# Kernel tuning notes

Hardware: AMD Instinct MI355X
Metric: run time of the kernel (lower is better)

## Reference

```python
import jax, jax.numpy as jnp
import numpy as np

S, B, H = 2048, 1, 1024
N_HEADS = 16
HEAD_DIM = H // N_HEADS
E, K, F = 8, 2, 2048  # experts, top_k, ffn_hidden
EPS = 1e-5


def layernorm(x, w, b):
    mu = jnp.mean(x, axis=-1, keepdims=True)
    var = jnp.mean(jnp.square(x - mu), axis=-1, keepdims=True)
    return (x - mu) * jax.lax.rsqrt(var + EPS) * w + b


def setup_inputs() -> dict:
    key = jax.random.key(0)
    ks = jax.random.split(key, 8)
    std = 0.02
    return {
        "x": jax.random.normal(ks[0], (S, B, H), dtype=jnp.float32),
        "ln1_w": jnp.ones((H,), jnp.float32),
        "ln1_b": jnp.zeros((H,), jnp.float32),
        "in_proj_w": jax.random.normal(ks[1], (3 * H, H), jnp.float32) * std,
        "in_proj_b": jnp.zeros((3 * H,), jnp.float32),
        "out_proj_w": jax.random.normal(ks[2], (H, H), jnp.float32) * std,
        "out_proj_b": jnp.zeros((H,), jnp.float32),
        "ln2_w": jnp.ones((H,), jnp.float32),
        "ln2_b": jnp.zeros((H,), jnp.float32),
        "router_w": jax.random.normal(ks[3], (E, H), jnp.float32) * std,
        "w1": jax.random.normal(ks[4], (E, H, F), jnp.float32) * std,
        "w2": jax.random.normal(ks[5], (E, F, H), jnp.float32) * std,
    }


def reference(x, ln1_w, ln1_b, in_proj_w, in_proj_b, out_proj_w, out_proj_b,
              ln2_w, ln2_b, router_w, w1, w2):
    s, b, h = x.shape
    # ---- causal self-attention (nn.MultiheadAttention math) ----
    hn = layernorm(x, ln1_w, ln1_b)
    qkv = hn @ in_proj_w.T + in_proj_b          # [S,B,3H]
    q, k, v = jnp.split(qkv, 3, axis=-1)
    q = q.reshape(s, b, N_HEADS, HEAD_DIM)
    k = k.reshape(s, b, N_HEADS, HEAD_DIM)
    v = v.reshape(s, b, N_HEADS, HEAD_DIM)
    scores = jnp.einsum('sbnd,tbnd->bnst', q, k) / np.sqrt(HEAD_DIM)
    causal = jnp.tril(jnp.ones((s, s), bool))
    scores = jnp.where(causal[None, None], scores, -jnp.inf)
    probs = jax.nn.softmax(scores, axis=-1)
    attn = jnp.einsum('bnst,tbnd->sbnd', probs, v).reshape(s, b, h)
    attn = attn @ out_proj_w.T + out_proj_b
    x1 = x + attn
    # ---- dMoE FFN: router softmax -> top-k gates -> expert GELU MLP ----
    hn2 = layernorm(x1, ln2_w, ln2_b).reshape(s * b, h)   # tokens [T,H]
    logits = hn2 @ router_w.T                              # [T,E]
    rp = jax.nn.softmax(logits, axis=-1)
    topw, topi = jax.lax.top_k(rp, K)                      # [T,K]
    gates = jnp.sum(jax.nn.one_hot(topi, E, dtype=hn2.dtype) * topw[..., None], axis=1)  # [T,E]
    hmid = jax.nn.gelu(jnp.einsum('th,ehf->tef', hn2, w1), approximate=False)  # [T,E,F]
    y = jnp.einsum('tef,efh->th', hmid * gates[:, :, None], w2)                # [T,H]
    return x1 + y.reshape(s, b, h)
```

## Files before the change

### kernel.cpp

```cpp
#include <hip/hip_runtime.h>

#define SL 2048
#define HID 1024
#define NHEAD 16
#define HD 64
#define NEXP 8
#define FF 2048
#define MAXTILE 40
#define MAXROWS (MAXTILE * 128)
#define CPAD 32

typedef short bf16x8 __attribute__((ext_vector_type(8)));
typedef float f32x4 __attribute__((ext_vector_type(4)));
typedef unsigned u32x4 __attribute__((ext_vector_type(4)));

__device__ __forceinline__ unsigned short f2bf(float f) {
  unsigned u = __builtin_bit_cast(unsigned, f);
  u += 0x7fffu + ((u >> 16) & 1u);
  return (unsigned short)(u >> 16);
}

__device__ __forceinline__ void gload16(const void* g, void* l) {
  __builtin_amdgcn_global_load_lds((const __attribute__((address_space(1))) void*)g,
                                   (__attribute__((address_space(3))) void*)l,
                                   16, 0, 0);
}

__device__ __forceinline__ void xcd_remap(int& bx, int& by) {
  const int nx = gridDim.x;
  const int nwg = nx * gridDim.y;
  const int L = by * nx + bx;
  const int per = nwg >> 3;
  const int Lp = (L & 7) * per + (L >> 3);
  bx = Lp % nx;
  by = Lp / nx;
}


#define PIPE_WAIT(i, NT)                                                     \
  if ((i) == (NT) - 1)                                                       \
    asm volatile("s_waitcnt vmcnt(0) lgkmcnt(0)" ::: "memory");              \
  else                                                                       \
    asm volatile("s_waitcnt vmcnt(4) lgkmcnt(0)" ::: "memory");              \
  __builtin_amdgcn_s_barrier();

#define GEMM_FRAGS_MFMA(CC)                                                  \
  bf16x8 af[4], bfr[4];                                                      \
  _Pragma("unroll")                                                          \
  for (int mt = 0; mt < 4; mt++)                                             \
    af[mt] = *reinterpret_cast<const bf16x8*>(                               \
        &Asm[CC][(wm + mt * 16 + la) * 32 + lk]);                            \
  _Pragma("unroll")                                                          \
  for (int nt = 0; nt < 4; nt++)                                             \
    bfr[nt] = *reinterpret_cast<const bf16x8*>(                              \
        &Bsm[CC][(wn + nt * 16 + la) * 32 + lk]);                            \
  __builtin_amdgcn_s_setprio(1);                                             \
  _Pragma("unroll")                                                          \
  for (int mt = 0; mt < 4; mt++)                                             \
    _Pragma("unroll")                                                        \
    for (int nt = 0; nt < 4; nt++)                                           \
      acc[mt][nt] =                                                          \
          __builtin_amdgcn_mfma_f32_16x16x32_bf16(af[mt], bfr[nt], acc[mt][nt], 0, 0, 0); \
  __builtin_amdgcn_s_setprio(0);

#define PIPE_ROT()                                                           \
  cc = (cc == 2) ? 0 : cc + 1;                                               \
  cs = (cs == 2) ? 0 : cs + 1;

template <int MODE>
__global__ __launch_bounds__(256) void gemm_bt(
    const unsigned short* __restrict__ A, const unsigned short* __restrict__ Bt,
    int M, int N, int Kstride, int Kloop,
    const float* __restrict__ bias,
    float* __restrict__ outf,
    unsigned short* __restrict__ q_out, unsigned short* __restrict__ k_out,
    unsigned short* __restrict__ vt_out)
{
  __shared__ unsigned short Asm[3][128 * 32];
  __shared__ unsigned short Bsm[3][128 * 32];
  int bx = blockIdx.x, by = blockIdx.y;
  xcd_remap(bx, by);
  const int tid = threadIdx.x;
  const int wave = tid >> 6;
  const int lane = tid & 63;
  const int m0 = by * 128;
  const int n0 = bx * 128;
  const int koff = blockIdx.z * Kloop;
  const int wm = (wave >> 1) * 64;
  const int wn = (wave & 1) * 64;
  const int la = lane & 15;
  const int lk = (lane >> 4) * 8;

  f32x4 acc[4][4] = {};

  const int srow = tid >> 2;
  const int skoff = (tid & 3) * 8;
  const unsigned short* Ag = A + (size_t)(m0 + srow) * Kstride + koff + skoff;
  const unsigned short* Bg = Bt + (size_t)(n0 + srow) * Kstride + koff + skoff;

  auto stage = [&](int s, int k0) {
    gload16(Ag + k0, &Asm[s][wave * 512]);
    gload16(Ag + (size_t)64 * Kstride + k0, &Asm[s][2048 + wave * 512]);
    gload16(Bg + k0, &Bsm[s][wave * 512]);
    gload16(Bg + (size_t)64 * Kstride + k0, &Bsm[s][2048 + wave * 512]);
  };

  stage(0, 0);
  stage(1, 32);
  const int NT = Kloop >> 5;
  int cc = 0, cs = 2;
  for (int i = 0; i < NT; ++i) {
    PIPE_WAIT(i, NT)
    if (i + 2 < NT) stage(cs, (i + 2) << 5);
    GEMM_FRAGS_MFMA(cc)
    PIPE_ROT()
  }

  const int lg = lane >> 4;
#pragma unroll
  for (int mt = 0; mt < 4; mt++) {
#pragma unroll
    for (int nt = 0; nt < 4; nt++) {
#pragma unroll
      for (int r = 0; r < 4; r++) {
        const int row = m0 + wm + mt * 16 + lg * 4 + r;
        const int col = n0 + wn + nt * 16 + la;
        float v = acc[mt][nt][r];
        if (MODE == 0) {
          v += bias[col];
          const int hh = (col & 1023) >> 6;
          const int dd = col & 63;
          const unsigned short bv = f2bf(v);
          if (col < 1024)
            q_out[(size_t)hh * SL * HD + (size_t)row * HD + dd] = bv;
          else if (col < 2048)
            k_out[(size_t)hh * SL * HD + (size_t)row * HD + dd] = bv;
          else
            vt_out[(size_t)hh * HD * SL + (size_t)dd * SL + row] = bv;
        } else {
          outf[(size_t)blockIdx.z * SL * HID + (size_t)row * HID + col] = v;
        }
      }
    }
  }
}

__global__ __launch_bounds__(256) void gemm_moe1(
    const unsigned short* __restrict__ A, const unsigned short* __restrict__ w1t,
    const int* __restrict__ perm, const float* __restrict__ gateg,
    const int* __restrict__ texp, const int* __restrict__ trow,
    unsigned short* __restrict__ hmidg)
{
  __shared__ unsigned short Asm[3][128 * 32];
  __shared__ unsigned short Bsm[3][128 * 32];
  int bx = blockIdx.x, by = blockIdx.y;
  xcd_remap(bx, by);
  const int e = texp[by];
  if (e < 0) return;
  const int row0 = trow[by];
  const int tid = threadIdx.x;
  const int wave = tid >> 6;
  const int lane = tid & 63;
  const int n0 = bx * 128;
  const int wm = (wave >> 1) * 64;
  const int wn = (wave & 1) * 64;
  const int la = lane & 15;
  const int lk = (lane >> 4) * 8;
  f32x4 acc[4][4] = {};

  const int srow = tid >> 2;
  const int skoff = (tid & 3) * 8;
  const int p0 = perm[row0 + srow];
  const int p1 = perm[row0 + 64 + srow];
  const unsigned short* Ag0 = A + (size_t)(p0 < 0 ? 0 : (p0 >> 1)) * HID + skoff;
  const unsigned short* Ag1 = A + (size_t)(p1 < 0 ? 0 : (p1 >> 1)) * HID + skoff;
  const unsigned short* Bg = w1t + (size_t)e * HID * FF + (size_t)(n0 + srow) * HID + skoff;

  auto stage = [&](int s, int k0) {
    gload16(Ag0 + k0, &Asm[s][wave * 512]);
    gload16(Ag1 + k0, &Asm[s][2048 + wave * 512]);
    gload16(Bg + k0, &Bsm[s][wave * 512]);
    gload16(Bg + (size_t)64 * HID + k0, &Bsm[s][2048 + wave * 512]);
  };

  stage(0, 0);
  stage(1, 32);
  const int NT = HID >> 5;
  int cc = 0, cs = 2;
  for (int i = 0; i < NT; ++i) {
    PIPE_WAIT(i, NT)
    if (i + 2 < NT) stage(cs, (i + 2) << 5);
    GEMM_FRAGS_MFMA(cc)
    PIPE_ROT()
  }

  const int lg = lane >> 4;
#pragma unroll
  for (int mt = 0; mt < 4; mt++) {
    float gr[4];
#pragma unroll
    for (int r = 0; r < 4; r++) gr[r] = gateg[row0 + wm + mt * 16 + lg * 4 + r];
#pragma unroll
    for (int nt = 0; nt < 4; nt++) {
#pragma unroll
      for (int r = 0; r < 4; r++) {
        const int grow = row0 + wm + mt * 16 + lg * 4 + r;
        const int col = n0 + wn + nt * 16 + la;
        const float v = acc[mt][nt][r];
        const float g = 0.5f * v * (1.0f + erff(v * 0.70710678118f));
        hmidg[(size_t)grow * FF + col] = f2bf(g * gr[r]);
      }
    }
  }
}

__global__ __launch_bounds__(256) void gemm_moe2(
    const unsigned short* __restrict__ A, const unsigned short* __restrict__ w2t,
    const int* __restrict__ perm,
    const int* __restrict__ texp, const int* __restrict__ trow,
    float* __restrict__ ybuf)
{
  __shared__ unsigned short Asm[3][128 * 32];
  __shared__ unsigned short Bsm[3][128 * 32];
  int bx = blockIdx.x, by = blockIdx.y;
  xcd_remap(bx, by);
  const int e = texp[by];
  if (e < 0) return;
  const int row0 = trow[by];
  const int tid = threadIdx.x;
  const int wave = tid >> 6;
  const int lane = tid & 63;
  const int n0 = bx * 128;
  const int koff = blockIdx.z * (FF / 2);
  const int wm = (wave >> 1) * 64;
  const int wn = (wave & 1) * 64;
  const int la = lane & 15;
  const int lk = (lane >> 4) * 8;
  f32x4 acc[4][4] = {};

  const int srow = tid >> 2;
  const int skoff = (tid & 3) * 8;
  const unsigned short* Ag = A + (size_t)(row0 + srow) * FF + koff + skoff;
  const unsigned short* Bg = w2t + (size_t)e * FF * HID + (size_t)(n0 + srow) * FF + koff + skoff;

  auto stage = [&](int s, int k0) {
    gload16(Ag + k0, &Asm[s][wave * 512]);
    gload16(Ag + (size_t)64 * FF + k0, &Asm[s][2048 + wave * 512]);
    gload16(Bg + k0, &Bsm[s][wave * 512]);
    gload16(Bg + (size_t)64 * FF + k0, &Bsm[s][2048 + wave * 512]);
  };

  stage(0, 0);
  stage(1, 32);
  const int NT = (FF / 2) >> 5;
  int cc = 0, cs = 2;
  for (int i = 0; i < NT; ++i) {
    PIPE_WAIT(i, NT)
    if (i + 2 < NT) stage(cs, (i + 2) << 5);
    GEMM_FRAGS_MFMA(cc)
    PIPE_ROT()
  }

  const int lg = lane >> 4;
#pragma unroll
  for (int mt = 0; mt < 4; mt++) {
    int pr[4];
#pragma unroll
    for (int r = 0; r < 4; r++) pr[r] = perm[row0 + wm + mt * 16 + lg * 4 + r];
#pragma unroll
    for (int nt = 0; nt < 4; nt++) {
#pragma unroll
      for (int r = 0; r < 4; r++) {
        const int p = pr[r];
        if (p >= 0) {
          const int col = n0 + wn + nt * 16 + la;
          ybuf[(size_t)(blockIdx.z * 2 + (p & 1)) * SL * HID + (size_t)(p >> 1) * HID + col] =
              acc[mt][nt][r];
        }
      }
    }
  }
}

__global__ __launch_bounds__(256) void ln_kernel(
    const float* __restrict__ x, const float* __restrict__ w, const float* __restrict__ b,
    unsigned short* __restrict__ ob)
{
  const int row = blockIdx.x;
  const int tid = threadIdx.x;
  const float4 v = *reinterpret_cast<const float4*>(&x[(size_t)row * HID + tid * 4]);
  float s = v.x + v.y + v.z + v.w;
  float q = v.x * v.x + v.y * v.y + v.z * v.z + v.w * v.w;
  for (int off = 32; off > 0; off >>= 1) {
    s += __shfl_down(s, off);
    q += __shfl_down(q, off);
  }
  __shared__ float ps[4], pq[4];
  const int wave = tid >> 6, lane = tid & 63;
  if (lane == 0) { ps[wave] = s; pq[wave] = q; }
  __syncthreads();
  s = ps[0] + ps[1] + ps[2] + ps[3];
  q = pq[0] + pq[1] + pq[2] + pq[3];
  const float mu = s * (1.0f / HID);
  const float inv = rsqrtf(q * (1.0f / HID) - mu * mu + 1e-5f);
  const int i = tid * 4;
  const float4 wv = *reinterpret_cast<const float4*>(&w[i]);
  const float4 bv = *reinterpret_cast<const float4*>(&b[i]);
  ushort4 u;
  u.x = f2bf((v.x - mu) * inv * wv.x + bv.x);
  u.y = f2bf((v.y - mu) * inv * wv.y + bv.y);
  u.z = f2bf((v.z - mu) * inv * wv.z + bv.z);
  u.w = f2bf((v.w - mu) * inv * wv.w + bv.w);
  *reinterpret_cast<ushort4*>(&ob[(size_t)row * HID + i]) = u;
}

__global__ __launch_bounds__(256) void combine_ln(
    const float4* __restrict__ x, const float* __restrict__ bias,
    const float4* __restrict__ p0, const float4* __restrict__ p1,
    float4* __restrict__ x1,
    const float* __restrict__ w, const float* __restrict__ b,
    unsigned short* __restrict__ ob, float* __restrict__ of)
{
  const int row = blockIdx.x;
  const int tid = threadIdx.x;
  const int i4 = row * 256 + tid;
  const int i = tid * 4;
  const float4 bv0 = *reinterpret_cast<const float4*>(&bias[i]);
  const float4 a = x[i4], c = p0[i4], d = p1[i4];
  float4 v;
  v.x = a.x + bv0.x + c.x + d.x;
  v.y = a.y + bv0.y + c.y + d.y;
  v.z = a.z + bv0.z + c.z + d.z;
  v.w = a.w + bv0.w + c.w + d.w;
  x1[i4] = v;
  float s = v.x + v.y + v.z + v.w;
  float q = v.x * v.x + v.y * v.y + v.z * v.z + v.w * v.w;
  for (int off = 32; off > 0; off >>= 1) {
    s += __shfl_down(s, off);
    q += __shfl_down(q, off);
  }
  __shared__ float ps[4], pq[4];
  const int wave = tid >> 6, lane = tid & 63;
  if (lane == 0) { ps[wave] = s; pq[wave] = q; }
  __syncthreads();
  s = ps[0] + ps[1] + ps[2] + ps[3];
  q = pq[0] + pq[1] + pq[2] + pq[3];
  const float mu = s * (1.0f / HID);
  const float inv = rsqrtf(q * (1.0f / HID) - mu * mu + 1e-5f);
  const float4 wv = *reinterpret_cast<const float4*>(&w[i]);
  const float4 bv = *reinterpret_cast<const float4*>(&b[i]);
  const float o0 = (v.x - mu) * inv * wv.x + bv.x;
  const float o1 = (v.y - mu) * inv * wv.y + bv.y;
  const float o2 = (v.z - mu) * inv * wv.z + bv.z;
  const float o3 = (v.w - mu) * inv * wv.w + bv.w;
  ushort4 u; u.x = f2bf(o0); u.y = f2bf(o1); u.z = f2bf(o2); u.w = f2bf(o3);
  *reinterpret_cast<ushort4*>(&ob[(size_t)row * HID + i]) = u;
  float4 o; o.x = o0; o.y = o1; o.z = o2; o.w = o3;
  *reinterpret_cast<float4*>(&of[(size_t)row * HID + i]) = o;
}

__global__ __launch_bounds__(256) void transpose_all(
    const float* __restrict__ w1, const float* __restrict__ w2,
    unsigned short* __restrict__ w1t, unsigned short* __restrict__ w2t)
{
  __shared__ float t[64][65];
  const int z = blockIdx.z;
  const float* in;
  unsigned short* out;
  int R, C, r0, c0;
  if (z < 8) {
    in = w1 + (size_t)z * HID * FF;  out = w1t + (size_t)z * HID * FF;
    R = HID; C = FF;  r0 = blockIdx.y * 64;  c0 = blockIdx.x * 64;
  } else {
    in = w2 + (size_t)(z - 8) * FF * HID;  out = w2t + (size_t)(z - 8) * FF * HID;
    R = FF; C = HID;  r0 = blockIdx.x * 64;  c0 = blockIdx.y * 64;
  }
  const int tid = threadIdx.x;
#pragma unroll
  for (int it = 0; it < 4; it++) {
    const int idx = it * 256 + tid;
    const int r = idx >> 4, c4 = (idx & 15) * 4;
    const float4 v = *reinterpret_cast<const float4*>(&in[(size_t)(r0 + r) * C + c0 + c4]);
    t[r][c4] = v.x; t[r][c4 + 1] = v.y; t[r][c4 + 2] = v.z; t[r][c4 + 3] = v.w;
  }
  __syncthreads();
#pragma unroll
  for (int it = 0; it < 4; it++) {
    const int idx = it * 256 + tid;
    const int c = idx >> 4, r4 = (idx & 15) * 4;
    ushort4 u;
    u.x = f2bf(t[r4][c]); u.y = f2bf(t[r4 + 1][c]);
    u.z = f2bf(t[r4 + 2][c]); u.w = f2bf(t[r4 + 3][c]);
    *reinterpret_cast<ushort4*>(&out[(size_t)(c0 + c) * R + r0 + r4]) = u;
  }
}

__global__ __launch_bounds__(256) void conv_bf16_2(
    const float4* __restrict__ a, const float4* __restrict__ b,
    ushort4* __restrict__ oa, ushort4* __restrict__ ob, int na4, int nb4)
{
  const int i = blockIdx.x * 256 + threadIdx.x;
  if (i < na4) {
    const float4 v = a[i];
    ushort4 u; u.x = f2bf(v.x); u.y = f2bf(v.y); u.z = f2bf(v.z); u.w = f2bf(v.w);
    oa[i] = u;
  } else if (i - na4 < nb4) {
    const float4 v = b[i - na4];
    ushort4 u; u.x = f2bf(v.x); u.y = f2bf(v.y); u.z = f2bf(v.z); u.w = f2bf(v.w);
    ob[i - na4] = u;
  }
}

__global__ __launch_bounds__(256) void router_kernel(
    const float* __restrict__ hn2f, const float* __restrict__ rw,
    int* __restrict__ ti, float* __restrict__ tg, int* __restrict__ cnt)
{
  __shared__ float wlds[NEXP * HID];
  __shared__ int lcnt[NEXP];
  const int tid = threadIdx.x;
#pragma unroll
  for (int i = 0; i < 8; i++)
    *reinterpret_cast<float4*>(&wlds[i * 1024 + tid * 4]) =
        *reinterpret_cast<const float4*>(&rw[i * 1024 + tid * 4]);
  if (tid < NEXP) lcnt[tid] = 0;
  __syncthreads();

  const int wave = tid >> 6, lane = tid & 63;
#pragma unroll 1
  for (int k = 0; k < 4; k++) {
    const int t = blockIdx.x * 16 + wave * 4 + k;
    float4 xr[4];
#pragma unroll
    for (int c = 0; c < 4; c++)
      xr[c] = *reinterpret_cast<const float4*>(&hn2f[(size_t)t * HID + c * 256 + lane * 4]);
    float p[NEXP];
#pragma unroll
    for (int e = 0; e < NEXP; e++) {
      float s = 0.f;
#pragma unroll
      for (int c = 0; c < 4; c++) {
        const float4 wv = *reinterpret_cast<const float4*>(&wlds[e * 1024 + c * 256 + lane * 4]);
        s += xr[c].x * wv.x + xr[c].y * wv.y + xr[c].z * wv.z + xr[c].w * wv.w;
      }
      s += __shfl_xor(s, 32);
      s += __shfl_xor(s, 16);
      s += __shfl_xor(s, 8);
      s += __shfl_xor(s, 4);
      s += __shfl_xor(s, 2);
      s += __shfl_xor(s, 1);
      p[e] = s;
    }
    if (lane == 0) {
      float mx = p[0];
#pragma unroll
      for (int e = 1; e < NEXP; e++) mx = fmaxf(mx, p[e]);
      float Z = 0.f;
#pragma unroll
      for (int e = 0; e < NEXP; e++) { p[e] = expf(p[e] - mx); Z += p[e]; }
      const float invZ = 1.f / Z;
      int i1 = 0;
#pragma unroll
      for (int e = 1; e < NEXP; e++) if (p[e] > p[i1]) i1 = e;
      int i2 = (i1 == 0) ? 1 : 0;
#pragma unroll
      for (int e = 0; e < NEXP; e++) if (e != i1 && p[e] > p[i2]) i2 = e;
      ti[2 * t] = i1; ti[2 * t + 1] = i2;
      tg[2 * t] = p[i1] * invZ; tg[2 * t + 1] = p[i2] * invZ;
      atomicAdd(&lcnt[i1], 1);
      atomicAdd(&lcnt[i2], 1);
    }
  }
  __syncthreads();
  if (tid < NEXP && lcnt[tid] > 0) atomicAdd(&cnt[tid * CPAD], lcnt[tid]);
}

__global__ void scan_kernel(const int* __restrict__ cnt, int* __restrict__ poff,
                            int* __restrict__ texp, int* __restrict__ trow)
{
  if (threadIdx.x == 0 && blockIdx.x == 0) {
    int off = 0, nt = 0;
    for (int e = 0; e < NEXP; e++) {
      poff[e] = off;
      const int c = cnt[e * CPAD];
      const int ntl = (c + 127) >> 7;
      for (int i = 0; i < ntl; i++) { texp[nt] = e; trow[nt] = off + i * 128; nt++; }
      off += ntl * 128;
    }
    for (int i = nt; i < MAXTILE; i++) { texp[i] = -1; trow[i] = 0; }
  }
}

__global__ __launch_bounds__(256) void build_kernel(
    const int* __restrict__ ti, const float* __restrict__ tg,
    const int* __restrict__ poff, int* __restrict__ fill,
    int* __restrict__ perm, float* __restrict__ gateg)
{
  __shared__ int lcnt[NEXP], lbase[NEXP];
  const int tid = threadIdx.x;
  if (tid < NEXP) lcnt[tid] = 0;
  __syncthreads();
  const int t = blockIdx.x * 256 + tid;
  int e0 = ti[2 * t], e1 = ti[2 * t + 1];
  int l0 = atomicAdd(&lcnt[e0], 1);
  int l1 = atomicAdd(&lcnt[e1], 1);
  __syncthreads();
  if (tid < NEXP) lbase[tid] = (lcnt[tid] > 0) ? atomicAdd(&fill[tid * CPAD], lcnt[tid]) : 0;
  __syncthreads();
  int pos0 = poff[e0] + lbase[e0] + l0;
  int pos1 = poff[e1] + lbase[e1] + l1;
  perm[pos0] = 2 * t;
  gateg[pos0] = tg[2 * t];
  perm[pos1] = 2 * t + 1;
  gateg[pos1] = tg[2 * t + 1];
}

__global__ __launch_bounds__(256) void final_add(
    const float4* __restrict__ x1, const float4* __restrict__ y0,
    const float4* __restrict__ y1, const float4* __restrict__ y2,
    const float4* __restrict__ y3, float4* __restrict__ out)
{
  const int i = blockIdx.x * 256 + threadIdx.x;
  const float4 a = x1[i], b = y0[i], c = y1[i], d = y2[i], e = y3[i];
  float4 o;
  o.x = a.x + b.x + c.x + d.x + e.x;
  o.y = a.y + b.y + c.y + d.y + e.y;
  o.z = a.z + b.z + c.z + d.z + e.z;
  o.w = a.w + b.w + c.w + d.w + e.w;
  out[i] = o;
}

#define SC2 0.1803368801111204f
#define PPITCH 20
__global__ __launch_bounds__(512) void attn_kernel(
    const unsigned short* __restrict__ qb, const unsigned short* __restrict__ kb,
    const unsigned short* __restrict__ vtb, unsigned short* __restrict__ attn)
{
  const int h = blockIdx.y;
  const int tid = threadIdx.x;
  const int wave = tid >> 6, lane = tid & 63;
  const int grp = wave >> 2;
  const int w4 = wave & 3;
  const int la = lane & 15, lg = lane >> 4;
  const int la7 = la & 7;
  __shared__ unsigned short Kt[2][2][64 * 64];
  __shared__ unsigned short Vt[2][2][64 * 64];
  __shared__ unsigned plds[8 * 32 * PPITCH];
  const unsigned short* qh = qb + (size_t)h * SL * HD;
  const unsigned short* kh = kb + (size_t)h * SL * HD;
  const unsigned short* vh = vtb + (size_t)h * HD * SL;
  unsigned* pu = &plds[wave * 32 * PPITCH];

  const int sr_lo = w4 * 8 + (lane >> 3);
  const int ss = lane & 7;

  auto stageKV = [&](int t, int buf) {
    const int kvb = t * 64;
#pragma unroll
    for (int j = 0; j < 2; j++) {
      const int row = j * 32 + sr_lo;
      const int s = ss ^ (row & 7);
      gload16(kh + (size_t)(kvb + row) * HD + s * 8, &Kt[grp][buf][j * 2048 + w4 * 512]);
      gload16(vh + (size_t)row * SL + kvb + s * 8, &Vt[grp][buf][j * 2048 + w4 * 512]);
    }
  };

  for (int half = 0; half < 2; half++) {
    const int qt = half ? (31 - blockIdx.x) : blockIdx.x;
    const int m0 = qt * 64 + w4 * 16;
    const int T = qt + 1;
    const int S = (T + 1) >> 1;
    const int q = m0 + la;

    bf16x8 aq0 = *reinterpret_cast<const bf16x8*>(&qh[(size_t)(m0 + la) * HD + lg * 8]);
    bf16x8 aq1 = *reinterpret_cast<const bf16x8*>(&qh[(size_t)(m0 + la) * HD + 32 + lg * 8]);

    f32x4 oacc[4] = {};
    float mrun = -1e30f, lrun = 0.f;

    if (grp < T) stageKV(grp, 0);
    __syncthreads();
    int cur = 0;

    for (int s = 0; s < S; s++) {
      const int tmy = 2 * s + grp;
      if (tmy + 2 < T) stageKV(tmy + 2, cur ^ 1);
      if (tmy < T) {
        const int kv0 = tmy * 64;
        const unsigned short* Kb = Kt[grp][cur];
        const unsigned short* Vb = Vt[grp][cur];

        f32x4 sac[4] = {};
        __builtin_amdgcn_s_setprio(1);
#pragma unroll
        for (int nt = 0; nt < 4; nt++) {
          const int row = nt * 16 + la;
          bf16x8 b0 = *reinterpret_cast<const bf16x8*>(&Kb[row * 64 + ((lg ^ la7) << 3)]);
          bf16x8 b1 = *reinterpret_cast<const bf16x8*>(&Kb[row * 64 + (((4 + lg) ^ la7) << 3)]);
          sac[nt] = __builtin_amdgcn_mfma_f32_16x16x32_bf16(b0, aq0, sac[nt], 0, 0, 0);
          sac[nt] = __builtin_amdgcn_mfma_f32_16x16x32_bf16(b1, aq1, sac[nt], 0, 0, 0);
        }
        __builtin_amdgcn_s_setprio(0);
        float sv[4][4];
        const bool diag = (tmy == qt);
#pragma unroll
        for (int nt = 0; nt < 4; nt++)
#pragma unroll
          for (int r = 0; r < 4; r++) {
            float xs = sac[nt][r] * SC2;
            if (diag && (kv0 + nt * 16 + lg * 4 + r) > q) xs = -1e30f;
            sv[nt][r] = xs;
          }
        float pm = fmaxf(fmaxf(sv[0][0], sv[0][1]), fmaxf(sv[0][2], sv[0][3]));
#pragma unroll
        for (int nt = 1; nt < 4; nt++)
          pm = fmaxf(pm, fmaxf(fmaxf(sv[nt][0], sv[nt][1]), fmaxf(sv[nt][2], sv[nt][3])));
        pm = fmaxf(pm, __shfl_xor(pm, 16));
        pm = fmaxf(pm, __shfl_xor(pm, 32));
        const float mn = fmaxf(mrun, pm);
        float rs = 0.f;
#pragma unroll
        for (int nt = 0; nt < 4; nt++)
#pragma unroll
          for (int r = 0; r < 4; r++) {
            const float pe = exp2f(sv[nt][r] - mn);
            sv[nt][r] = pe;
            rs += pe;
          }
        rs += __shfl_xor(rs, 16);
        rs += __shfl_xor(rs, 32);
        if (__ballot(pm > mrun) != 0ULL) {
          const float al = exp2f(mrun - mn);
#pragma unroll
          for (int dt = 0; dt < 4; dt++)
#pragma unroll
            for (int r = 0; r < 4; r++) oacc[dt][r] *= al;
          lrun = lrun * al + rs;
          mrun = mn;
        } else {
          lrun += rs;
        }
#pragma unroll
        for (int nt = 0; nt < 4; nt++)
#pragma unroll
          for (int rp = 0; rp < 2; rp++) {
            unsigned pk;
            asm("v_cvt_pk_bf16_f32 %0, %1, %2"
                : "=v"(pk) : "v"(sv[nt][rp * 2]), "v"(sv[nt][rp * 2 + 1]));
            pu[(nt * 8 + lg * 2 + rp) * PPITCH + la] = pk;
          }
        asm volatile("s_waitcnt lgkmcnt(0)" ::: "memory");
        __builtin_amdgcn_sched_barrier(0);
        u32x4 w0, w1;
#pragma unroll
        for (int jj = 0; jj < 4; jj++) {
          w0[jj] = pu[(lg * 4 + jj) * PPITCH + la];
          w1[jj] = pu[(16 + lg * 4 + jj) * PPITCH + la];
        }
        const bf16x8 pa0 = __builtin_bit_cast(bf16x8, w0);
        const bf16x8 pa1 = __builtin_bit_cast(bf16x8, w1);
        __builtin_amdgcn_s_setprio(1);
#pragma unroll
        for (int dt = 0; dt < 4; dt++) {
          const int row = dt * 16 + la;
          bf16x8 v0 = *reinterpret_cast<const bf16x8*>(&Vb[row * 64 + ((lg ^ la7) << 3)]);
          bf16x8 v1 = *reinterpret_cast<const bf16x8*>(&Vb[row * 64 + (((4 + lg) ^ la7) << 3)]);
          oacc[dt] = __builtin_amdgcn_mfma_f32_16x16x32_bf16(v0, pa0, oacc[dt], 0, 0, 0);
          oacc[dt] = __builtin_amdgcn_mfma_f32_16x16x32_bf16(v1, pa1, oacc[dt], 0, 0, 0);
        }
        __builtin_amdgcn_s_setprio(0);
      }
      __syncthreads();
      cur ^= 1;
    }

    float* xb = (float*)&Kt[0][0][0];
    float* mlb = (float*)&Vt[0][0][0];
    if (grp == 1) {
#pragma unroll
      for (int dt = 0; dt < 4; dt++)
#pragma unroll
        for (int r = 0; r < 4; r++)
          xb[w4 * 1024 + (dt * 16 + lg * 4 + r) * 16 + la] = oacc[dt][r];
      if (lg == 0) {
        mlb[w4 * 32 + la * 2] = mrun;
        mlb[w4 * 32 + la * 2 + 1] = lrun;
      }
    }
    __syncthreads();
    if (grp == 0) {
      const float m1 = mlb[w4 * 32 + la * 2];
      const float l1 = mlb[w4 * 32 + la * 2 + 1];
      const float mm = fmaxf(mrun, m1);
      const float a0 = exp2f(mrun - mm);
      const float a1 = exp2f(m1 - mm);
      const float linv = 1.0f / (lrun * a0 + l1 * a1);
#pragma unroll
      for (int dt = 0; dt < 4; dt++) {
        ushort4 u;
        float o0 = (oacc[dt][0] * a0 + xb[w4 * 1024 + (dt * 16 + lg * 4 + 0) * 16 + la] * a1) * linv;
        float o1 = (oacc[dt][1] * a0 + xb[w4 * 1024 + (dt * 16 + lg * 4 + 1) * 16 + la] * a1) * linv;
        float o2 = (oacc[dt][2] * a0 + xb[w4 * 1024 + (dt * 16 + lg * 4 + 2) * 16 + la] * a1) * linv;
        float o3 = (oacc[dt][3] * a0 + xb[w4 * 1024 + (dt * 16 + lg * 4 + 3) * 16 + la] * a1) * linv;
        u.x = f2bf(o0); u.y = f2bf(o1); u.z = f2bf(o2); u.w = f2bf(o3);
        *reinterpret_cast<ushort4*>(&attn[(size_t)q * HID + h * HD + dt * 16 + lg * 4]) = u;
      }
    }
    __syncthreads();
  }
}

extern "C" void kernel_launch(void* const* d_in, const int* in_sizes, int n_in,
                              void* d_out, int out_size, void* d_ws, size_t ws_size,
                              hipStream_t stream)
{
  const float* x          = (const float*)d_in[0];
  const float* ln1_w      = (const float*)d_in[1];
  const float* ln1_b      = (const float*)d_in[2];
  const float* in_proj_w  = (const float*)d_in[3];
  const float* in_proj_b  = (const float*)d_in[4];
  const float* out_proj_w = (const float*)d_in[5];
  const float* out_proj_b = (const float*)d_in[6];
  const float* ln2_w      = (const float*)d_in[7];
  const float* ln2_b      = (const float*)d_in[8];
  const float* router_w   = (const float*)d_in[9];
  const float* w1         = (const float*)d_in[10];
  const float* w2         = (const float*)d_in[11];
  float* out = (float*)d_out;

  char* ws = (char*)d_ws;
  size_t off = 0;
  auto alloc = [&](size_t bytes) -> void* {
    void* p = ws + off;
    off += (bytes + 255) & ~(size_t)255;
    return p;
  };
  unsigned short* hn_b   = (unsigned short*)alloc((size_t)SL * HID * 2);
  unsigned short* ipw_b  = (unsigned short*)alloc((size_t)3 * HID * HID * 2);
  unsigned short* opw_b  = (unsigned short*)alloc((size_t)HID * HID * 2);
  unsigned short* qb     = (unsigned short*)alloc((size_t)SL * HID * 2);
  unsigned short* kb     = (unsigned short*)alloc((size_t)SL * HID * 2);
  unsigned short* vtb    = (unsigned short*)alloc((size_t)SL * HID * 2);
  unsigned short* attn_b = (unsigned short*)alloc((size_t)SL * HID * 2);
  float*          x1     = (float*)alloc((size_t)SL * HID * 4);
  float*          pbuf   = (float*)alloc((size_t)2 * SL * HID * 4);
  unsigned short* hn2_b  = (unsigned short*)alloc((size_t)SL * HID * 2);
  float*          hn2_f  = (float*)alloc((size_t)SL * HID * 4);
  unsigned short* w1t    = (unsigned short*)alloc((size_t)NEXP * HID * FF * 2);
  unsigned short* w2t    = (unsigned short*)alloc((size_t)NEXP * HID * FF * 2);
  unsigned short* hmidg  = (unsigned short*)alloc((size_t)MAXROWS * FF * 2);
  float*          ybuf   = (float*)alloc((size_t)4 * SL * HID * 4);
  int*            ti     = (int*)alloc((size_t)SL * 2 * 4);
  float*          tg     = (float*)alloc((size_t)SL * 2 * 4);
  int*            perm   = (int*)alloc((size_t)MAXROWS * 4);
  float*          gateg  = (float*)alloc((size_t)MAXROWS * 4);
  int*            cnt    = (int*)alloc(NEXP * CPAD * 4);
  int*            fill   = (int*)alloc(NEXP * CPAD * 4);
  int*            poff   = (int*)alloc(64 * 4);
  int*            texp   = (int*)alloc(64 * 4);
  int*            trow   = (int*)alloc(64 * 4);

  const dim3 blk(256);

  hipMemsetAsync(cnt, 0, NEXP * CPAD * 4, stream);
  hipMemsetAsync(fill, 0, NEXP * CPAD * 4, stream);
  hipMemsetAsync(perm, 0xFF, (size_t)MAXROWS * 4, stream);
  hipMemsetAsync(gateg, 0, (size_t)MAXROWS * 4, stream);

  conv_bf16_2<<<4096, blk, 0, stream>>>(
      (const float4*)in_proj_w, (const float4*)out_proj_w,
      (ushort4*)ipw_b, (ushort4*)opw_b, 3 * HID * HID / 4, HID * HID / 4);
  transpose_all<<<dim3(32, 16, 16), blk, 0, stream>>>(w1, w2, w1t, w2t);

  ln_kernel<<<SL, blk, 0, stream>>>(x, ln1_w, ln1_b, hn_b);

  gemm_bt<0><<<dim3(3 * HID / 128, SL / 128), blk, 0, stream>>>(
      hn_b, ipw_b, SL, 3 * HID, HID, HID,
      in_proj_b, nullptr, qb, kb, vtb);

  attn_kernel<<<dim3(16, NHEAD), dim3(512), 0, stream>>>(qb, kb, vtb, attn_b);

  gemm_bt<2><<<dim3(HID / 128, SL / 128, 2), blk, 0, stream>>>(
      attn_b, opw_b, SL, HID, HID, HID / 2,
      nullptr, pbuf, nullptr, nullptr, nullptr);

  combine_ln<<<SL, blk, 0, stream>>>(
      (const float4*)x, out_proj_b, (const float4*)pbuf,
      (const float4*)(pbuf + (size_t)SL * HID), (float4*)x1,
      ln2_w, ln2_b, hn2_b, hn2_f);

  router_kernel<<<SL / 16, blk, 0, stream>>>(hn2_f, router_w, ti, tg, cnt);
  scan_kernel<<<1, 64, 0, stream>>>(cnt, poff, texp, trow);
  build_kernel<<<SL / 256, blk, 0, stream>>>(ti, tg, poff, fill, perm, gateg);

  gemm_moe1<<<dim3(FF / 128, MAXTILE), blk, 0, stream>>>(
      hn2_b, w1t, perm, gateg, texp, trow, hmidg);
  gemm_moe2<<<dim3(HID / 128, MAXTILE, 2), blk, 0, stream>>>(
      hmidg, w2t, perm, texp, trow, ybuf);

  final_add<<<SL * HID / 1024, blk, 0, stream>>>(
      (const float4*)x1, (const float4*)ybuf,
      (const float4*)(ybuf + (size_t)SL * HID),
      (const float4*)(ybuf + (size_t)2 * SL * HID),
      (const float4*)(ybuf + (size_t)3 * SL * HID),
      (float4*)out);
}
```

Measured before the change: 263.4 us.

## Fuse expert weight transpose and bf16 conversion into MoE GEMM B-tile staging

```diff
diff --git a/kernel.cpp b/kernel.cpp
--- a/kernel.cpp
+++ b/kernel.cpp
@@ -9,6 +9,7 @@
 #define MAXTILE 40
 #define MAXROWS (MAXTILE * 128)
 #define CPAD 32
+#define BPITCH 36
 
 typedef short bf16x8 __attribute__((ext_vector_type(8)));
 typedef float f32x4 __attribute__((ext_vector_type(4)));
@@ -35,7 +36,6 @@
   bx = Lp % nx;
   by = Lp / nx;
 }
-
 
 #define PIPE_WAIT(i, NT)                                                     \
   if ((i) == (NT) - 1)                                                       \
@@ -145,14 +145,40 @@
   }
 }
 
+
+__device__ __forceinline__ bf16x8 bfragB(const unsigned short* Bu, int n, int lk) {
+  const uint2 lo = *reinterpret_cast<const uint2*>(&Bu[n * BPITCH + lk]);
+  const uint2 hi = *reinterpret_cast<const uint2*>(&Bu[n * BPITCH + lk + 4]);
+  u32x4 w; w[0] = lo.x; w[1] = lo.y; w[2] = hi.x; w[3] = hi.y;
+  return __builtin_bit_cast(bf16x8, w);
+}
+
+#define MOE_FRAGS_MFMA(CC)                                                   \
+  bf16x8 af[4], bfr[4];                                                      \
+  _Pragma("unroll")                                                          \
+  for (int mt = 0; mt < 4; mt++)                                             \
+    af[mt] = *reinterpret_cast<const bf16x8*>(                               \
+        &Asm[CC][(wm + mt * 16 + la) * 32 + lk]);                            \
+  _Pragma("unroll")                                                          \
+  for (int nt = 0; nt < 4; nt++)                                             \
+    bfr[nt] = bfragB(BsmU[CC], wn + nt * 16 + la, lk);                       \
+  __builtin_amdgcn_s_setprio(1);                                             \
+  _Pragma("unroll")                                                          \
+  for (int mt = 0; mt < 4; mt++)                                             \
+    _Pragma("unroll")                                                        \
+    for (int nt = 0; nt < 4; nt++)                                           \
+      acc[mt][nt] =                                                          \
+          __builtin_amdgcn_mfma_f32_16x16x32_bf16(af[mt], bfr[nt], acc[mt][nt], 0, 0, 0); \
+  __builtin_amdgcn_s_setprio(0);
+
 __global__ __launch_bounds__(256) void gemm_moe1(
-    const unsigned short* __restrict__ A, const unsigned short* __restrict__ w1t,
+    const unsigned short* __restrict__ A, const float* __restrict__ w1,
     const int* __restrict__ perm, const float* __restrict__ gateg,
     const int* __restrict__ texp, const int* __restrict__ trow,
     unsigned short* __restrict__ hmidg)
 {
-  __shared__ unsigned short Asm[3][128 * 32];
-  __shared__ unsigned short Bsm[3][128 * 32];
+  __shared__ unsigned short Asm[2][128 * 32];
+  __shared__ unsigned short BsmU[2][128 * BPITCH];
   int bx = blockIdx.x, by = blockIdx.y;
   xcd_remap(bx, by);
   const int e = texp[by];
@@ -174,24 +200,37 @@
   const int p1 = perm[row0 + 64 + srow];
   const unsigned short* Ag0 = A + (size_t)(p0 < 0 ? 0 : (p0 >> 1)) * HID + skoff;
   const unsigned short* Ag1 = A + (size_t)(p1 < 0 ? 0 : (p1 >> 1)) * HID + skoff;
-  const unsigned short* Bg = w1t + (size_t)e * HID * FF + (size_t)(n0 + srow) * HID + skoff;
-
-  auto stage = [&](int s, int k0) {
-    gload16(Ag0 + k0, &Asm[s][wave * 512]);
-    gload16(Ag1 + k0, &Asm[s][2048 + wave * 512]);
-    gload16(Bg + k0, &Bsm[s][wave * 512]);
-    gload16(Bg + (size_t)64 * HID + k0, &Bsm[s][2048 + wave * 512]);
+  const float* Bf = w1 + (size_t)e * HID * FF + n0;
+  const int sc = tid & 31;
+  const int skr = tid >> 5;
+
+  auto stageA = [&](int buf, int k0) {
+    gload16(Ag0 + k0, &Asm[buf][wave * 512]);
+    gload16(Ag1 + k0, &Asm[buf][2048 + wave * 512]);
   };
-
-  stage(0, 0);
-  stage(1, 32);
-  const int NT = HID >> 5;
-  int cc = 0, cs = 2;
-  for (int i = 0; i < NT; ++i) {
-    PIPE_WAIT(i, NT)
-    if (i + 2 < NT) stage(cs, (i + 2) << 5);
-    GEMM_FRAGS_MFMA(cc)
-    PIPE_ROT()
+  auto stageB = [&](int buf, int k0) {
+#pragma unroll
+    for (int p = 0; p < 4; p++) {
+      const int k = p * 8 + skr;
+      const float* src = Bf + (size_t)(k0 + k) * FF + sc;
+#pragma unroll
+      for (int j = 0; j < 4; j++)
+        BsmU[buf][(sc + 32 * j) * BPITCH + k] = f2bf(src[32 * j]);
+    }
+  };
+
+  stageA(0, 0);
+  stageB(0, 0);
+  __syncthreads();
+  int cur = 0;
+  for (int k0 = 0; k0 < HID; k0 += 32) {
+    if (k0 + 32 < HID) {
+      stageA(cur ^ 1, k0 + 32);
+      stageB(cur ^ 1, k0 + 32);
+    }
+    MOE_FRAGS_MFMA(cur)
+    __syncthreads();
+    cur ^= 1;
   }
 
   const int lg = lane >> 4;
@@ -215,13 +254,13 @@
 }
 
 __global__ __launch_bounds__(256) void gemm_moe2(
-    const unsigned short* __restrict__ A, const unsigned short* __restrict__ w2t,
+    const unsigned short* __restrict__ A, const float* __restrict__ w2,
     const int* __restrict__ perm,
     const int* __restrict__ texp, const int* __restrict__ trow,
     float* __restrict__ ybuf)
 {
-  __shared__ unsigned short Asm[3][128 * 32];
-  __shared__ unsigned short Bsm[3][128 * 32];
+  __shared__ unsigned short Asm[2][128 * 32];
+  __shared__ unsigned short BsmU[2][128 * BPITCH];
   int bx = blockIdx.x, by = blockIdx.y;
   xcd_remap(bx, by);
   const int e = texp[by];
@@ -241,24 +280,37 @@
   const int srow = tid >> 2;
   const int skoff = (tid & 3) * 8;
   const unsigned short* Ag = A + (size_t)(row0 + srow) * FF + koff + skoff;
-  const unsigned short* Bg = w2t + (size_t)e * FF * HID + (size_t)(n0 + srow) * FF + koff + skoff;
-
-  auto stage = [&](int s, int k0) {
-    gload16(Ag + k0, &Asm[s][wave * 512]);
-    gload16(Ag + (size_t)64 * FF + k0, &Asm[s][2048 + wave * 512]);
-    gload16(Bg + k0, &Bsm[s][wave * 512]);
-    gload16(Bg + (size_t)64 * FF + k0, &Bsm[s][2048 + wave * 512]);
+  const float* Bf = w2 + (size_t)e * FF * HID + (size_t)koff * HID + n0;
+  const int sc = tid & 31;
+  const int skr = tid >> 5;
+
+  auto stageA = [&](int buf, int k0) {
+    gload16(Ag + k0, &Asm[buf][wave * 512]);
+    gload16(Ag + (size_t)64 * FF + k0, &Asm[buf][2048 + wave * 512]);
   };
-
-  stage(0, 0);
-  stage(1, 32);
-  const int NT = (FF / 2) >> 5;
-  int cc = 0, cs = 2;
-  for (int i = 0; i < NT; ++i) {
-    PIPE_WAIT(i, NT)
-    if (i + 2 < NT) stage(cs, (i + 2) << 5);
-    GEMM_FRAGS_MFMA(cc)
-    PIPE_ROT()
+  auto stageB = [&](int buf, int k0) {
+#pragma unroll
+    for (int p = 0; p < 4; p++) {
+      const int k = p * 8 + skr;
+      const float* src = Bf + (size_t)(k0 + k) * HID + sc;
+#pragma unroll
+      for (int j = 0; j < 4; j++)
+        BsmU[buf][(sc + 32 * j) * BPITCH + k] = f2bf(src[32 * j]);
+    }
+  };
+
+  stageA(0, 0);
+  stageB(0, 0);
+  __syncthreads();
+  int cur = 0;
+  for (int k0 = 0; k0 < FF / 2; k0 += 32) {
+    if (k0 + 32 < FF / 2) {
+      stageA(cur ^ 1, k0 + 32);
+      stageB(cur ^ 1, k0 + 32);
+    }
+    MOE_FRAGS_MFMA(cur)
+    __syncthreads();
+    cur ^= 1;
   }
 
   const int lg = lane >> 4;
@@ -359,42 +411,6 @@
   *reinterpret_cast<float4*>(&of[(size_t)row * HID + i]) = o;
 }
 
-__global__ __launch_bounds__(256) void transpose_all(
-    const float* __restrict__ w1, const float* __restrict__ w2,
-    unsigned short* __restrict__ w1t, unsigned short* __restrict__ w2t)
-{
-  __shared__ float t[64][65];
-  const int z = blockIdx.z;
-  const float* in;
-  unsigned short* out;
-  int R, C, r0, c0;
-  if (z < 8) {
-    in = w1 + (size_t)z * HID * FF;  out = w1t + (size_t)z * HID * FF;
-    R = HID; C = FF;  r0 = blockIdx.y * 64;  c0 = blockIdx.x * 64;
-  } else {
-    in = w2 + (size_t)(z - 8) * FF * HID;  out = w2t + (size_t)(z - 8) * FF * HID;
-    R = FF; C = HID;  r0 = blockIdx.x * 64;  c0 = blockIdx.y * 64;
-  }
-  const int tid = threadIdx.x;
-#pragma unroll
-  for (int it = 0; it < 4; it++) {
-    const int idx = it * 256 + tid;
-    const int r = idx >> 4, c4 = (idx & 15) * 4;
-    const float4 v = *reinterpret_cast<const float4*>(&in[(size_t)(r0 + r) * C + c0 + c4]);
-    t[r][c4] = v.x; t[r][c4 + 1] = v.y; t[r][c4 + 2] = v.z; t[r][c4 + 3] = v.w;
-  }
-  __syncthreads();
-#pragma unroll
-  for (int it = 0; it < 4; it++) {
-    const int idx = it * 256 + tid;
-    const int c = idx >> 4, r4 = (idx & 15) * 4;
-    ushort4 u;
-    u.x = f2bf(t[r4][c]); u.y = f2bf(t[r4 + 1][c]);
-    u.z = f2bf(t[r4 + 2][c]); u.w = f2bf(t[r4 + 3][c]);
-    *reinterpret_cast<ushort4*>(&out[(size_t)(c0 + c) * R + r0 + r4]) = u;
-  }
-}
-
 __global__ __launch_bounds__(256) void conv_bf16_2(
     const float4* __restrict__ a, const float4* __restrict__ b,
     ushort4* __restrict__ oa, ushort4* __restrict__ ob, int na4, int nb4)
@@ -745,8 +761,6 @@
   float*          pbuf   = (float*)alloc((size_t)2 * SL * HID * 4);
   unsigned short* hn2_b  = (unsigned short*)alloc((size_t)SL * HID * 2);
   float*          hn2_f  = (float*)alloc((size_t)SL * HID * 4);
-  unsigned short* w1t    = (unsigned short*)alloc((size_t)NEXP * HID * FF * 2);
-  unsigned short* w2t    = (unsigned short*)alloc((size_t)NEXP * HID * FF * 2);
   unsigned short* hmidg  = (unsigned short*)alloc((size_t)MAXROWS * FF * 2);
   float*          ybuf   = (float*)alloc((size_t)4 * SL * HID * 4);
   int*            ti     = (int*)alloc((size_t)SL * 2 * 4);
@@ -769,7 +783,6 @@
   conv_bf16_2<<<4096, blk, 0, stream>>>(
       (const float4*)in_proj_w, (const float4*)out_proj_w,
       (ushort4*)ipw_b, (ushort4*)opw_b, 3 * HID * HID / 4, HID * HID / 4);
-  transpose_all<<<dim3(32, 16, 16), blk, 0, stream>>>(w1, w2, w1t, w2t);
 
   ln_kernel<<<SL, blk, 0, stream>>>(x, ln1_w, ln1_b, hn_b);
 
@@ -793,9 +806,9 @@
   build_kernel<<<SL / 256, blk, 0, stream>>>(ti, tg, poff, fill, perm, gateg);
 
   gemm_moe1<<<dim3(FF / 128, MAXTILE), blk, 0, stream>>>(
-      hn2_b, w1t, perm, gateg, texp, trow, hmidg);
+      hn2_b, w1, perm, gateg, texp, trow, hmidg);
   gemm_moe2<<<dim3(HID / 128, MAXTILE, 2), blk, 0, stream>>>(
-      hmidg, w2t, perm, texp, trow, ybuf);
+      hmidg, w2, perm, texp, trow, ybuf);
 
   final_add<<<SL * HID / 1024, blk, 0, stream>>>(
       (const float4*)x1, (const float4*)ybuf,
```

After: 261.2 us. Within noise of the previous version (-0.8%).
